# Kernel optimization log

Measured on AMD Instinct MI355X. Metric: run time of the kernel, lower is better.

## Reference

```python
import jax, jax.numpy as jnp
import numpy as np

TOP_K = 5
THRESHOLD = 0.0
EPS = 1e-12

def l2_normalize(x, axis):
    sq = jnp.sum(x * x, axis=axis, keepdims=True)
    return x * jax.lax.rsqrt(jnp.maximum(sq, EPS))

def setup_inputs() -> dict:
    key = jax.random.key(0)
    k1, k2, k3, k4 = jax.random.split(key, 4)
    B, S, D = 256, 197, 768
    P, L, T = 20, 5, 10
    x_embed = jax.random.normal(k1, (B, S, D), dtype=jnp.float32)
    prompt = jax.random.uniform(k2, (P, L, D), dtype=jnp.float32, minval=-1.0, maxval=1.0)
    prompt_key = jax.random.uniform(k3, (P, D), dtype=jnp.float32, minval=-1.0, maxval=1.0)
    assist_prompt = jax.random.uniform(k4, (T, L, D), dtype=jnp.float32, minval=-1.0, maxval=1.0)
    return {"x_embed": x_embed, "prompt": prompt, "prompt_key": prompt_key,
            "assist_prompt": assist_prompt, "test": 0}

def reference(x_embed, prompt, prompt_key, assist_prompt, test):
    B = x_embed.shape[0]
    D = x_embed.shape[-1]
    # embedding key: mean over tokens
    x_mean = jnp.mean(x_embed, axis=1)                 # [B, D]
    x_norm = l2_normalize(x_mean, axis=1)              # [B, D]  (test >= 0 branch)
    p_norm = l2_normalize(prompt_key, axis=1)          # [P, D]
    similarity = x_norm @ p_norm.T                     # [B, P]
    vals, idx = jax.lax.top_k(similarity, TOP_K)       # sorted descending -> pruning mask is a prefix
    keep = vals > THRESHOLD                            # [B, K]
    idx_pruned = jnp.where(keep, idx, -1)              # [B, K], -1 = dummy prompt
    idx_safe = jnp.maximum(idx_pruned, 0)
    # gather selected prompts, zero-out pruned slots (dummy prompts)
    sel = jnp.where(keep[:, :, None, None], prompt[idx_safe], 0.0)     # [B, K, L, D]
    assist_b = jnp.broadcast_to(assist_prompt, (B,) + assist_prompt.shape)  # [B, T, L, D]
    selected = jnp.concatenate([assist_b, sel], axis=1)                # [B, T+K, L, D]
    tokens = selected.reshape(B, -1, D)                                # [B, (T+K)*L, D]
    # reduce_sim: sum over all valid (b,k) keys of key . x_b', summed over b', / B
    gathered_keys = jnp.where(keep[:, :, None], p_norm[idx_safe], 0.0) # [B, K, D]
    key_total = jnp.sum(gathered_keys, axis=(0, 1))                    # [D]
    reduce_sim = jnp.dot(jnp.sum(x_norm, axis=0), key_total) / B
    prompted_embedding = jnp.concatenate([tokens, x_embed], axis=1)    # [B, (T+K)*L + S, D]
    return prompted_embedding, reduce_sim, tokens, idx_pruned, x_norm
```

## Files before the change

kernel.cpp:

```cpp
#include <hip/hip_runtime.h>

#define B 256
#define S 197
#define D 768
#define P 20
#define L 5
#define T 10
#define K 5

#define ROWS_PE 272
#define SZ_PE   (B * ROWS_PE * D)
#define OFF_RS  ((long)SZ_PE)
#define OFF_TOK (OFF_RS + 1)
#define SZ_TOK  (B * (T + K) * L * D)
#define OFF_IDX (OFF_TOK + SZ_TOK)
#define OFF_XN  (OFF_IDX + B * K)

__global__ void k_mean_copy(const float* __restrict__ x, float* __restrict__ pe,
                            float* __restrict__ partial) {
    const int tile = blockIdx.x;
    const int b = blockIdx.y;
    const int t = threadIdx.x;
    const int s0 = tile * 50;
    const int s1 = (s0 + 50 < S) ? s0 + 50 : S;
    const float4* x4 = (const float4*)x;
    float4* o4 = (float4*)pe;
    const int xbase = (b * S) * (D / 4) + t;
    const int obase = (b * ROWS_PE + (T + K) * L) * (D / 4) + t;
    float4 acc = make_float4(0.f, 0.f, 0.f, 0.f);
    for (int s = s0; s < s1; ++s) {
        float4 v = x4[xbase + s * (D / 4)];
        acc.x += v.x; acc.y += v.y; acc.z += v.z; acc.w += v.w;
        o4[obase + s * (D / 4)] = v;
    }
    ((float4*)partial)[(b * 4 + tile) * (D / 4) + t] = acc;
}

__global__ void k_norm(const float* __restrict__ partial, const float* __restrict__ pkey,
                       float* __restrict__ xnorm_out, float* __restrict__ pnorm) {
    const int blk = blockIdx.x;
    const int t = threadIdx.x;
    float v0, v1, v2;
    if (blk < B) {
        v0 = v1 = v2 = 0.f;
        for (int tile = 0; tile < 4; ++tile) {
            const float* p = partial + (blk * 4 + tile) * D;
            v0 += p[t]; v1 += p[t + 256]; v2 += p[t + 512];
        }
        const float invS = 1.0f / (float)S;
        v0 *= invS; v1 *= invS; v2 *= invS;
    } else {
        const float* p = pkey + (blk - B) * D;
        v0 = p[t]; v1 = p[t + 256]; v2 = p[t + 512];
    }
    float ss = v0 * v0 + v1 * v1 + v2 * v2;
    for (int o = 32; o > 0; o >>= 1) ss += __shfl_down(ss, o);
    __shared__ float red[4];
    const int lane = t & 63, wid = t >> 6;
    if (lane == 0) red[wid] = ss;
    __syncthreads();
    if (t == 0) {
        float s = red[0] + red[1] + red[2] + red[3];
        red[0] = rsqrtf(fmaxf(s, 1e-12f));
    }
    __syncthreads();
    const float r = red[0];
    float* dst = (blk < B) ? (xnorm_out + blk * D) : (pnorm + (blk - B) * D);
    dst[t] = v0 * r; dst[t + 256] = v1 * r; dst[t + 512] = v2 * r;
}

__global__ void k_simtopk(const float* __restrict__ xnorm, const float* __restrict__ pnorm,
                          float* __restrict__ idxp_f, int* __restrict__ idx_ws,
                          int* __restrict__ keycnt) {
    const int b = blockIdx.x;
    const int t = threadIdx.x;
    __shared__ float xs[D];
    __shared__ float sim[P];
    xs[t] = xnorm[b * D + t];
    xs[t + 256] = xnorm[b * D + t + 256];
    xs[t + 512] = xnorm[b * D + t + 512];
    __syncthreads();
    const int wid = t >> 6, lane = t & 63;
    for (int p = wid; p < P; p += 4) {
        float acc = 0.f;
        const float* pr = pnorm + p * D;
        for (int d = lane; d < D; d += 64) acc += xs[d] * pr[d];
        for (int o = 32; o > 0; o >>= 1) acc += __shfl_down(acc, o);
        if (lane == 0) sim[p] = acc;
    }
    __syncthreads();
    if (t == 0) {
        bool used[P];
        for (int p = 0; p < P; ++p) used[p] = false;
        for (int k = 0; k < K; ++k) {
            float best = -INFINITY; int bi = 0;
            for (int p = 0; p < P; ++p)
                if (!used[p] && sim[p] > best) { best = sim[p]; bi = p; }
            used[bi] = true;
            const int oi = (best > 0.0f) ? bi : -1;
            idxp_f[b * K + k] = (float)oi;
            idx_ws[b * K + k] = oi;
            if (oi >= 0) atomicAdd(&keycnt[bi], 1);
        }
    }
}

__global__ void k_tokens(const float* __restrict__ prompt, const float* __restrict__ assist,
                         const int* __restrict__ idx_ws, float* __restrict__ pe,
                         float* __restrict__ tok) {
    const int j = blockIdx.x;
    const int b = blockIdx.y;
    const int t = threadIdx.x;
    float v0, v1, v2;
    if (j < T * L) {
        const float* src = assist + j * D;
        v0 = src[t]; v1 = src[t + 256]; v2 = src[t + 512];
    } else {
        const int k = (j - T * L) / L, l = (j - T * L) % L;
        const int idx = idx_ws[b * K + k];
        if (idx < 0) {
            v0 = v1 = v2 = 0.f;
        } else {
            const float* src = prompt + (idx * L + l) * D;
            v0 = src[t]; v1 = src[t + 256]; v2 = src[t + 512];
        }
    }
    float* d1 = pe + (long)(b * ROWS_PE + j) * D;
    d1[t] = v0; d1[t + 256] = v1; d1[t + 512] = v2;
    float* d2 = tok + (long)(b * (T + K) * L + j) * D;
    d2[t] = v0; d2[t + 256] = v1; d2[t + 512] = v2;
}

__global__ void k_reduce(const float* __restrict__ xnorm, const float* __restrict__ pnorm,
                         const int* __restrict__ keycnt, float* __restrict__ rs) {
    const int t = threadIdx.x;
    __shared__ float cnt[P];
    if (t < P) cnt[t] = (float)keycnt[t];
    __syncthreads();
    float acc = 0.f;
    for (int c = 0; c < 3; ++c) {
        const int d = t + c * 256;
        float xsum = 0.f;
        for (int b = 0; b < B; ++b) xsum += xnorm[b * D + d];
        float kt = 0.f;
        for (int p = 0; p < P; ++p) kt += cnt[p] * pnorm[p * D + d];
        acc += xsum * kt;
    }
    for (int o = 32; o > 0; o >>= 1) acc += __shfl_down(acc, o);
    __shared__ float red[4];
    const int lane = t & 63, wid = t >> 6;
    if (lane == 0) red[wid] = acc;
    __syncthreads();
    if (t == 0) rs[0] = (red[0] + red[1] + red[2] + red[3]) * (1.0f / (float)B);
}

extern "C" void kernel_launch(void* const* d_in, const int* in_sizes, int n_in,
                              void* d_out, int out_size, void* d_ws, size_t ws_size,
                              hipStream_t stream) {
    const float* x      = (const float*)d_in[0];
    const float* prompt = (const float*)d_in[1];
    const float* pkey   = (const float*)d_in[2];
    const float* assist = (const float*)d_in[3];
    float* out = (float*)d_out;
    float* ws = (float*)d_ws;

    float* partial = ws;
    float* pnorm   = ws + B * 4 * D;
    int*   idx_ws  = (int*)(pnorm + P * D);
    int*   keycnt  = idx_ws + B * K;

    hipMemsetAsync(keycnt, 0, P * sizeof(int), stream);

    k_mean_copy<<<dim3(4, B), 192, 0, stream>>>(x, out, partial);
    k_norm<<<B + P, 256, 0, stream>>>(partial, pkey, out + OFF_XN, pnorm);
    k_simtopk<<<B, 256, 0, stream>>>(out + OFF_XN, pnorm, out + OFF_IDX, idx_ws, keycnt);
    k_tokens<<<dim3((T + K) * L, B), 256, 0, stream>>>(prompt, assist, idx_ws, out, out + OFF_TOK);
    k_reduce<<<1, 256, 0, stream>>>(out + OFF_XN, pnorm, keycnt, out + OFF_RS);
}
```

Before: 462.9 us.

## Fuse normalization into similarity/top-k kernel and accumulate x_norm sum atomically

Result: no change. 462.4 us (-0.1%).

```diff
diff --git a/kernel.cpp b/kernel.cpp
--- a/kernel.cpp
+++ b/kernel.cpp
@@ -36,57 +36,54 @@
     ((float4*)partial)[(b * 4 + tile) * (D / 4) + t] = acc;
 }
 
-__global__ void k_norm(const float* __restrict__ partial, const float* __restrict__ pkey,
-                       float* __restrict__ xnorm_out, float* __restrict__ pnorm) {
-    const int blk = blockIdx.x;
-    const int t = threadIdx.x;
-    float v0, v1, v2;
-    if (blk < B) {
-        v0 = v1 = v2 = 0.f;
-        for (int tile = 0; tile < 4; ++tile) {
-            const float* p = partial + (blk * 4 + tile) * D;
-            v0 += p[t]; v1 += p[t + 256]; v2 += p[t + 512];
-        }
-        const float invS = 1.0f / (float)S;
-        v0 *= invS; v1 *= invS; v2 *= invS;
-    } else {
-        const float* p = pkey + (blk - B) * D;
-        v0 = p[t]; v1 = p[t + 256]; v2 = p[t + 512];
-    }
-    float ss = v0 * v0 + v1 * v1 + v2 * v2;
-    for (int o = 32; o > 0; o >>= 1) ss += __shfl_down(ss, o);
-    __shared__ float red[4];
-    const int lane = t & 63, wid = t >> 6;
-    if (lane == 0) red[wid] = ss;
-    __syncthreads();
-    if (t == 0) {
-        float s = red[0] + red[1] + red[2] + red[3];
-        red[0] = rsqrtf(fmaxf(s, 1e-12f));
-    }
-    __syncthreads();
-    const float r = red[0];
-    float* dst = (blk < B) ? (xnorm_out + blk * D) : (pnorm + (blk - B) * D);
-    dst[t] = v0 * r; dst[t + 256] = v1 * r; dst[t + 512] = v2 * r;
-}
-
-__global__ void k_simtopk(const float* __restrict__ xnorm, const float* __restrict__ pnorm,
+__global__ void k_simtopk(const float* __restrict__ partial, const float* __restrict__ pkey,
+                          float* __restrict__ xnorm_out, float* __restrict__ xsum,
                           float* __restrict__ idxp_f, int* __restrict__ idx_ws,
                           int* __restrict__ keycnt) {
     const int b = blockIdx.x;
     const int t = threadIdx.x;
+    const int lane = t & 63, wid = t >> 6;
     __shared__ float xs[D];
     __shared__ float sim[P];
-    xs[t] = xnorm[b * D + t];
-    xs[t + 256] = xnorm[b * D + t + 256];
-    xs[t + 512] = xnorm[b * D + t + 512];
+    __shared__ float red[4];
+
+    float v0 = 0.f, v1 = 0.f, v2 = 0.f;
+    for (int tile = 0; tile < 4; ++tile) {
+        const float* p = partial + (b * 4 + tile) * D;
+        v0 += p[t]; v1 += p[t + 256]; v2 += p[t + 512];
+    }
+    const float invS = 1.0f / (float)S;
+    v0 *= invS; v1 *= invS; v2 *= invS;
+    float ss = v0 * v0 + v1 * v1 + v2 * v2;
+    for (int o = 32; o > 0; o >>= 1) ss += __shfl_down(ss, o);
+    if (lane == 0) red[wid] = ss;
     __syncthreads();
-    const int wid = t >> 6, lane = t & 63;
+    if (t == 0) red[0] = rsqrtf(fmaxf(red[0] + red[1] + red[2] + red[3], 1e-12f));
+    __syncthreads();
+    const float r = red[0];
+    v0 *= r; v1 *= r; v2 *= r;
+    xs[t] = v0; xs[t + 256] = v1; xs[t + 512] = v2;
+    xnorm_out[b * D + t] = v0;
+    xnorm_out[b * D + t + 256] = v1;
+    xnorm_out[b * D + t + 512] = v2;
+    atomicAdd(&xsum[t], v0);
+    atomicAdd(&xsum[t + 256], v1);
+    atomicAdd(&xsum[t + 512], v2);
+    __syncthreads();
+
     for (int p = wid; p < P; p += 4) {
-        float acc = 0.f;
-        const float* pr = pnorm + p * D;
-        for (int d = lane; d < D; d += 64) acc += xs[d] * pr[d];
-        for (int o = 32; o > 0; o >>= 1) acc += __shfl_down(acc, o);
-        if (lane == 0) sim[p] = acc;
+        const float* pr = pkey + p * D;
+        float axk = 0.f, akk = 0.f;
+        for (int d = lane; d < D; d += 64) {
+            const float kv = pr[d];
+            axk += xs[d] * kv;
+            akk += kv * kv;
+        }
+        for (int o = 32; o > 0; o >>= 1) {
+            axk += __shfl_down(axk, o);
+            akk += __shfl_down(akk, o);
+        }
+        if (lane == 0) sim[p] = axk * rsqrtf(fmaxf(akk, 1e-12f));
     }
     __syncthreads();
     if (t == 0) {
@@ -111,44 +108,42 @@
     const int j = blockIdx.x;
     const int b = blockIdx.y;
     const int t = threadIdx.x;
-    float v0, v1, v2;
+    float4 v;
     if (j < T * L) {
-        const float* src = assist + j * D;
-        v0 = src[t]; v1 = src[t + 256]; v2 = src[t + 512];
+        v = ((const float4*)(assist + j * D))[t];
     } else {
         const int k = (j - T * L) / L, l = (j - T * L) % L;
         const int idx = idx_ws[b * K + k];
-        if (idx < 0) {
-            v0 = v1 = v2 = 0.f;
-        } else {
-            const float* src = prompt + (idx * L + l) * D;
-            v0 = src[t]; v1 = src[t + 256]; v2 = src[t + 512];
-        }
+        if (idx < 0) v = make_float4(0.f, 0.f, 0.f, 0.f);
+        else         v = ((const float4*)(prompt + (idx * L + l) * D))[t];
     }
-    float* d1 = pe + (long)(b * ROWS_PE + j) * D;
-    d1[t] = v0; d1[t + 256] = v1; d1[t + 512] = v2;
-    float* d2 = tok + (long)(b * (T + K) * L + j) * D;
-    d2[t] = v0; d2[t + 256] = v1; d2[t + 512] = v2;
+    ((float4*)(pe + (long)(b * ROWS_PE + j) * D))[t] = v;
+    float* d2 = tok + (long)(b * (T + K) * L + j) * D + 4 * t;
+    d2[0] = v.x; d2[1] = v.y; d2[2] = v.z; d2[3] = v.w;
 }
 
-__global__ void k_reduce(const float* __restrict__ xnorm, const float* __restrict__ pnorm,
+__global__ void k_reduce(const float* __restrict__ xsum, const float* __restrict__ pkey,
                          const int* __restrict__ keycnt, float* __restrict__ rs) {
     const int t = threadIdx.x;
-    __shared__ float cnt[P];
-    if (t < P) cnt[t] = (float)keycnt[t];
+    const int lane = t & 63, wid = t >> 6;
+    __shared__ float coef[P];
+    __shared__ float red[4];
+    for (int p = wid; p < P; p += 4) {
+        const float* pr = pkey + p * D;
+        float akk = 0.f;
+        for (int d = lane; d < D; d += 64) { const float kv = pr[d]; akk += kv * kv; }
+        for (int o = 32; o > 0; o >>= 1) akk += __shfl_down(akk, o);
+        if (lane == 0) coef[p] = (float)keycnt[p] * rsqrtf(fmaxf(akk, 1e-12f));
+    }
     __syncthreads();
     float acc = 0.f;
     for (int c = 0; c < 3; ++c) {
         const int d = t + c * 256;
-        float xsum = 0.f;
-        for (int b = 0; b < B; ++b) xsum += xnorm[b * D + d];
         float kt = 0.f;
-        for (int p = 0; p < P; ++p) kt += cnt[p] * pnorm[p * D + d];
-        acc += xsum * kt;
+        for (int p = 0; p < P; ++p) kt += coef[p] * pkey[p * D + d];
+        acc += xsum[d] * kt;
     }
     for (int o = 32; o > 0; o >>= 1) acc += __shfl_down(acc, o);
-    __shared__ float red[4];
-    const int lane = t & 63, wid = t >> 6;
     if (lane == 0) red[wid] = acc;
     __syncthreads();
     if (t == 0) rs[0] = (red[0] + red[1] + red[2] + red[3]) * (1.0f / (float)B);
@@ -165,15 +160,15 @@
     float* ws = (float*)d_ws;
 
     float* partial = ws;
-    float* pnorm   = ws + B * 4 * D;
-    int*   idx_ws  = (int*)(pnorm + P * D);
-    int*   keycnt  = idx_ws + B * K;
+    int*   keycnt  = (int*)(partial + B * 4 * D);
+    float* xsum    = (float*)(keycnt + P);
+    int*   idx_ws  = (int*)(xsum + D);
 
-    hipMemsetAsync(keycnt, 0, P * sizeof(int), stream);
+    hipMemsetAsync(keycnt, 0, (P + D) * sizeof(float), stream);
 
     k_mean_copy<<<dim3(4, B), 192, 0, stream>>>(x, out, partial);
-    k_norm<<<B + P, 256, 0, stream>>>(partial, pkey, out + OFF_XN, pnorm);
-    k_simtopk<<<B, 256, 0, stream>>>(out + OFF_XN, pnorm, out + OFF_IDX, idx_ws, keycnt);
-    k_tokens<<<dim3((T + K) * L, B), 256, 0, stream>>>(prompt, assist, idx_ws, out, out + OFF_TOK);
-    k_reduce<<<1, 256, 0, stream>>>(out + OFF_XN, pnorm, keycnt, out + OFF_RS);
+    k_simtopk<<<B, 256, 0, stream>>>(partial, pkey, out + OFF_XN, xsum,
+                                     out + OFF_IDX, idx_ws, keycnt);
+    k_tokens<<<dim3((T + K) * L, B), 192, 0, stream>>>(prompt, assist, idx_ws, out, out + OFF_TOK);
+    k_reduce<<<1, 256, 0, stream>>>(xsum, pkey, keycnt, out + OFF_RS);
 }
```
